# Optimization experiments

Hardware: AMD Instinct MI355X
Metric: run time of the kernel (lower is better)

Reference implementation:

```python
import jax, jax.numpy as jnp
import numpy as np

B, S, D, H, L, V, C = 8, 1024, 768, 12, 6, 32000, 2
HD = D // H
DF = 3072
MAX_POS = 2048
EPS = 1e-5


def layer_norm(x, scale, bias):
    m = jnp.mean(x, axis=-1, keepdims=True)
    v = jnp.mean((x - m) ** 2, axis=-1, keepdims=True)
    return (x - m) / jnp.sqrt(v + EPS) * scale + bias


def setup_inputs() -> dict:
    key = jax.random.key(0)
    ks = jax.random.split(key, 16)
    std = 0.02
    return {
        "input_ids": jax.random.randint(ks[0], (B, S), 0, V),
        "attention_mask": jax.random.randint(ks[1], (B, S), 0, 2),
        "token_emb": jax.random.normal(ks[2], (V, D), jnp.float32) * std,
        "pos_emb": jax.random.normal(ks[3], (MAX_POS, D), jnp.float32) * std,
        "qkv_w": jax.random.normal(ks[4], (L, D, 3 * D), jnp.float32) * std,
        "qkv_b": jnp.zeros((L, 3 * D), jnp.float32),
        "out_w": jax.random.normal(ks[5], (L, D, D), jnp.float32) * std,
        "out_b": jnp.zeros((L, D), jnp.float32),
        "n1_s": jnp.ones((L, D), jnp.float32),
        "n1_b": jnp.zeros((L, D), jnp.float32),
        "ff1_w": jax.random.normal(ks[6], (L, D, DF), jnp.float32) * std,
        "ff1_b": jnp.zeros((L, DF), jnp.float32),
        "ff2_w": jax.random.normal(ks[7], (L, DF, D), jnp.float32) * std,
        "ff2_b": jnp.zeros((L, D), jnp.float32),
        "n2_s": jnp.ones((L, D), jnp.float32),
        "n2_b": jnp.zeros((L, D), jnp.float32),
        "hln_s": jnp.ones((D,), jnp.float32),
        "hln_b": jnp.zeros((D,), jnp.float32),
        "cls_w": jax.random.normal(ks[8], (D, C), jnp.float32) * std,
        "cls_b": jnp.zeros((C,), jnp.float32),
    }


def reference(input_ids, attention_mask, token_emb, pos_emb, qkv_w, qkv_b,
              out_w, out_b, n1_s, n1_b, ff1_w, ff1_b, ff2_w, ff2_b,
              n2_s, n2_b, hln_s, hln_b, cls_w, cls_b):
    # embeddings: token + position, scaled by sqrt(d_model)
    x = (token_emb[input_ids] + pos_emb[:S][None, :, :]) * np.float32(np.sqrt(D))
    # extended mask: 0 at valid tokens, -10000 at padding -> (B,1,1,S)
    ext = (1.0 - attention_mask.astype(x.dtype))[:, None, None, :] * -10000.0
    scale = np.float32(1.0 / np.sqrt(HD))
    for i in range(L):
        # --- self attention (pre-norm) ---
        h = layer_norm(x, n1_s[i], n1_b[i])
        qkv = (h @ qkv_w[i] + qkv_b[i]).reshape(B, S, H, 3, HD)
        q, k, v = qkv[..., 0, :], qkv[..., 1, :], qkv[..., 2, :]  # (B,S,H,HD)
        scores = jnp.einsum('bshd,bthd->bhst', q, k) * scale
        # faithful to source: masked_fill(ext_mask == 0, -1e9)
        scores = jnp.where(ext == 0, jnp.asarray(-1e9, scores.dtype), scores)
        w = jax.nn.softmax(scores, axis=-1)
        att = jnp.einsum('bhst,bthd->bshd', w, v).reshape(B, S, D)
        x = x + (att @ out_w[i] + out_b[i])
        # --- feed forward (pre-norm) ---
        h2 = layer_norm(x, n2_s[i], n2_b[i])
        ff = jax.nn.relu(h2 @ ff1_w[i] + ff1_b[i]) @ ff2_w[i] + ff2_b[i]
        x = x + ff
    # CLS pooling head
    pooled = layer_norm(x[:, 0, :], hln_s, hln_b)
    return pooled @ cls_w + cls_b
```

## Files before the change

kernel.cpp:

```cpp
#include <hip/hip_runtime.h>
#include <hip/hip_bf16.h>

typedef unsigned short u16;
typedef __bf16 bf16x8 __attribute__((ext_vector_type(8)));
typedef float f32x4 __attribute__((ext_vector_type(4)));
typedef unsigned int u32x4 __attribute__((ext_vector_type(4)));

#define DEVI __device__ __forceinline__

typedef __attribute__((address_space(3))) void lds_void;
typedef __attribute__((address_space(1))) const void gbl_void;

DEVI void gload16(const void* gp, void* lp) {
    __builtin_amdgcn_global_load_lds((gbl_void*)gp, (lds_void*)lp, 16, 0, 0);
}

DEVI u16 f2b(float f) {
    unsigned int u = __builtin_bit_cast(unsigned int, f);
    unsigned int lsb = (u >> 16) & 1u;
    u += 0x7fffu + lsb;
    return (u16)(u >> 16);
}
DEVI float b2f(u16 b) {
    unsigned int u = ((unsigned int)b) << 16;
    return __builtin_bit_cast(float, u);
}

DEVI float blockReduceSum(float v, float* red, int tid) {
    #pragma unroll
    for (int o = 32; o; o >>= 1) v += __shfl_xor(v, o);
    __syncthreads();
    if ((tid & 63) == 0) red[tid >> 6] = v;
    __syncthreads();
    return red[0] + red[1] + red[2] + red[3];
}

__global__ void detect_kernel(const void* tok, int* flag) {
    __shared__ int bad;
    if (threadIdx.x == 0) bad = 0;
    __syncthreads();
    const u16* p = (const u16*)tok;
    int cnt = 0;
    for (int j = 0; j < 16; ++j) {
        float v = b2f(p[2 * (threadIdx.x * 16 + j)]);
        if (!(fabsf(v) < 1.0f)) cnt++;
    }
    if (cnt) atomicAdd(&bad, 1);
    __syncthreads();
    if (threadIdx.x == 0) flag[0] = (bad == 0) ? 1 : 0;
}

__global__ void to_f32_kernel(const void* src, float* dst, int n, const int* flag) {
    int i = blockIdx.x * 256 + threadIdx.x;
    if (i >= n) return;
    if (flag[0]) dst[i] = b2f(((const u16*)src)[i]);
    else         dst[i] = ((const float*)src)[i];
}

DEVI void gemm_core_async(const u16* __restrict__ A, int lda,
                          const u16* __restrict__ Bt, int ldb,
                          int K, f32x4 (&acc)[4][4],
                          u16* As, u16* Bs)
{
    const int tid  = threadIdx.x;
    const int lane = tid & 63;
    const int wave = tid >> 6;
    const int quad = lane >> 4;
    const int l16  = lane & 15;
    const int wm   = wave >> 1;
    const int wn   = wave & 1;

    const int c0 = (wave * 2 + 0) * 64 + lane;
    const int c1 = (wave * 2 + 1) * 64 + lane;
    const int r0 = c0 >> 2, h0 = (c0 & 3) * 8;
    const int r1 = c1 >> 2, h1 = (c1 & 3) * 8;

    for (int k0 = 0; k0 < K; k0 += 32) {
        __syncthreads();
        gload16(A  + (size_t)r0 * lda + k0 + h0, As + c0 * 8);
        gload16(Bt + (size_t)r0 * ldb + k0 + h0, Bs + c0 * 8);
        gload16(A  + (size_t)r1 * lda + k0 + h1, As + c1 * 8);
        gload16(Bt + (size_t)r1 * ldb + k0 + h1, Bs + c1 * 8);
        __syncthreads();

        bf16x8 af[4], bfv[4];
        #pragma unroll
        for (int mt = 0; mt < 4; ++mt)
            af[mt] = *(const bf16x8*)(As + (wm * 64 + mt * 16 + l16) * 32 + quad * 8);
        #pragma unroll
        for (int nt = 0; nt < 4; ++nt)
            bfv[nt] = *(const bf16x8*)(Bs + (wn * 64 + nt * 16 + l16) * 32 + quad * 8);
        #pragma unroll
        for (int mt = 0; mt < 4; ++mt)
            #pragma unroll
            for (int nt = 0; nt < 4; ++nt)
                acc[mt][nt] = __builtin_amdgcn_mfma_f32_16x16x32_bf16(af[mt], bfv[nt], acc[mt][nt], 0, 0, 0);
    }
}

template<int EPI>
__global__ __launch_bounds__(256) void gemm_std(
    const u16* __restrict__ A, int lda,
    const u16* __restrict__ Bt, int ldb,
    const float* __restrict__ bias,
    u16* __restrict__ outB, int ldc, int K)
{
    __shared__ u16 As[128 * 32];
    __shared__ u16 Bs[128 * 32];
    const size_t bM = (size_t)blockIdx.y * 128;
    const size_t bN = (size_t)blockIdx.x * 128;
    f32x4 acc[4][4] = {};
    gemm_core_async(A + bM * lda, lda, Bt + bN * ldb, ldb, K, acc, As, Bs);

    const int tid = threadIdx.x, lane = tid & 63, wave = tid >> 6;
    const int wm = wave >> 1, wn = wave & 1, quad = lane >> 4, l16 = lane & 15;
    #pragma unroll
    for (int mt = 0; mt < 4; ++mt)
        #pragma unroll
        for (int nt = 0; nt < 4; ++nt) {
            size_t col = bN + wn * 64 + nt * 16 + l16;
            float bcol = bias[col];
            #pragma unroll
            for (int r = 0; r < 4; ++r) {
                size_t row = bM + wm * 64 + mt * 16 + quad * 4 + r;
                float v = acc[mt][nt][r] + bcol;
                if constexpr (EPI == 1) v = fmaxf(v, 0.f);
                outB[row * ldc + col] = f2b(v);
            }
        }
}

__global__ __launch_bounds__(256) void gemm_splitk(
    const u16* __restrict__ A, int lda,
    const u16* __restrict__ Bt, int ldb,
    const float* __restrict__ bias,
    float* __restrict__ resid, int ldc, int Ksub)
{
    __shared__ u16 As[128 * 32];
    __shared__ u16 Bs[128 * 32];
    const size_t bM = (size_t)blockIdx.y * 128;
    const size_t bN = (size_t)blockIdx.x * 128;
    const int Koff = blockIdx.z * Ksub;
    f32x4 acc[4][4] = {};
    gemm_core_async(A + bM * lda + Koff, lda, Bt + bN * ldb + Koff, ldb, Ksub, acc, As, Bs);

    const int tid = threadIdx.x, lane = tid & 63, wave = tid >> 6;
    const int wm = wave >> 1, wn = wave & 1, quad = lane >> 4, l16 = lane & 15;
    const bool addb = (blockIdx.z == 0);
    #pragma unroll
    for (int mt = 0; mt < 4; ++mt)
        #pragma unroll
        for (int nt = 0; nt < 4; ++nt) {
            size_t col = bN + wn * 64 + nt * 16 + l16;
            float bcol = addb ? bias[col] : 0.f;
            #pragma unroll
            for (int r = 0; r < 4; ++r) {
                size_t row = bM + wm * 64 + mt * 16 + quad * 4 + r;
                atomicAdd(&resid[row * ldc + col], acc[mt][nt][r] + bcol);
            }
        }
}

__global__ __launch_bounds__(256, 2) void flash_attn(
    const u16* __restrict__ qkv, const u16* __restrict__ vt,
    const int* __restrict__ mask, u16* __restrict__ attout)
{
    __shared__ u16 Ks[128 * 72];
    __shared__ u16 Vs[64 * 136];
    __shared__ u16 Ps[128 * 136];
    __shared__ float Ms[1024];

    const int bh = blockIdx.y;
    const int b = bh / 12, h = bh % 12;
    const int q0 = blockIdx.x * 128;
    const int tid = threadIdx.x, lane = tid & 63, wave = tid >> 6;
    const int quad = lane >> 4, l16 = lane & 15;

    for (int i = tid; i < 1024; i += 256)
        Ms[i] = (mask[b * 1024 + i] != 0) ? 1.f : 0.f;

    bf16x8 aq[2][2];
    #pragma unroll
    for (int mt = 0; mt < 2; ++mt)
        #pragma unroll
        for (int s = 0; s < 2; ++s)
            aq[mt][s] = *(const bf16x8*)(qkv + (size_t)(b * 1024 + q0 + wave * 32 + mt * 16 + l16) * 2304
                                          + h * 192 + s * 32 + quad * 8);

    float mi[2][4], li[2][4];
    f32x4 Oacc[2][4] = {};
    #pragma unroll
    for (int mt = 0; mt < 2; ++mt)
        #pragma unroll
        for (int r = 0; r < 4; ++r) { mi[mt][r] = -3e38f; li[mt][r] = 0.f; }

    for (int kt = 0; kt < 8; ++kt) {
        u32x4 kreg[4], vreg[4];
        #pragma unroll
        for (int i = 0; i < 4; ++i) {
            int id = i * 256 + tid, row = id >> 3, ch = id & 7;
            kreg[i] = *(const u32x4*)(qkv + (size_t)(b * 1024 + kt * 128 + row) * 2304 + h * 192 + 64 + ch * 8);
        }
        #pragma unroll
        for (int i = 0; i < 4; ++i) {
            int id = i * 256 + tid, row = id >> 4, ch = id & 15;
            vreg[i] = *(const u32x4*)(vt + (size_t)bh * 65536 + (size_t)row * 1024 + kt * 128 + ch * 8);
        }
        __syncthreads();
        #pragma unroll
        for (int i = 0; i < 4; ++i) {
            int id = i * 256 + tid, row = id >> 3, ch = id & 7;
            *(u32x4*)(Ks + row * 72 + ch * 8) = kreg[i];
        }
        #pragma unroll
        for (int i = 0; i < 4; ++i) {
            int id = i * 256 + tid, row = id >> 4, ch = id & 15;
            *(u32x4*)(Vs + row * 136 + ch * 8) = vreg[i];
        }
        __syncthreads();

        f32x4 Sacc[2][8] = {};
        #pragma unroll
        for (int s = 0; s < 2; ++s) {
            bf16x8 kf[8];
            #pragma unroll
            for (int nt = 0; nt < 8; ++nt)
                kf[nt] = *(const bf16x8*)(Ks + (nt * 16 + l16) * 72 + s * 32 + quad * 8);
            #pragma unroll
            for (int mt = 0; mt < 2; ++mt)
                #pragma unroll
                for (int nt = 0; nt < 8; ++nt)
                    Sacc[mt][nt] = __builtin_amdgcn_mfma_f32_16x16x32_bf16(aq[mt][s], kf[nt], Sacc[mt][nt], 0, 0, 0);
        }

        float mval[8];
        #pragma unroll
        for (int nt = 0; nt < 8; ++nt) mval[nt] = Ms[kt * 128 + nt * 16 + l16];
        #pragma unroll
        for (int mt = 0; mt < 2; ++mt)
            #pragma unroll
            for (int nt = 0; nt < 8; ++nt)
                #pragma unroll
                for (int r = 0; r < 4; ++r)
                    Sacc[mt][nt][r] = (mval[nt] != 0.f) ? -1e9f : Sacc[mt][nt][r] * 0.125f;

        #pragma unroll
        for (int mt = 0; mt < 2; ++mt) {
            float al[4];
            #pragma unroll
            for (int r = 0; r < 4; ++r) {
                float rm = -3e38f;
                #pragma unroll
                for (int nt = 0; nt < 8; ++nt) rm = fmaxf(rm, Sacc[mt][nt][r]);
                #pragma unroll
                for (int o = 8; o; o >>= 1) rm = fmaxf(rm, __shfl_xor(rm, o));
                float mn = fmaxf(mi[mt][r], rm);
                al[r] = __expf(mi[mt][r] - mn);
                mi[mt][r] = mn;
                float rs = 0.f;
                #pragma unroll
                for (int nt = 0; nt < 8; ++nt) {
                    float pv = __expf(Sacc[mt][nt][r] - mn);
                    rs += pv;
                    Sacc[mt][nt][r] = pv;
                }
                #pragma unroll
                for (int o = 8; o; o >>= 1) rs += __shfl_xor(rs, o);
                li[mt][r] = li[mt][r] * al[r] + rs;
            }
            #pragma unroll
            for (int ntv = 0; ntv < 4; ++ntv)
                #pragma unroll
                for (int r = 0; r < 4; ++r) Oacc[mt][ntv][r] *= al[r];
            const int rowb = wave * 32 + mt * 16 + quad * 4;
            #pragma unroll
            for (int nt = 0; nt < 8; ++nt)
                #pragma unroll
                for (int r = 0; r < 4; ++r)
                    Ps[(rowb + r) * 136 + nt * 16 + l16] = f2b(Sacc[mt][nt][r]);
        }

        #pragma unroll
        for (int s2 = 0; s2 < 4; ++s2) {
            bf16x8 vf[4];
            #pragma unroll
            for (int ntv = 0; ntv < 4; ++ntv)
                vf[ntv] = *(const bf16x8*)(Vs + (ntv * 16 + l16) * 136 + s2 * 32 + quad * 8);
            #pragma unroll
            for (int mt2 = 0; mt2 < 2; ++mt2) {
                bf16x8 pf = *(const bf16x8*)(Ps + (wave * 32 + mt2 * 16 + l16) * 136 + s2 * 32 + quad * 8);
                #pragma unroll
                for (int ntv = 0; ntv < 4; ++ntv)
                    Oacc[mt2][ntv] = __builtin_amdgcn_mfma_f32_16x16x32_bf16(pf, vf[ntv], Oacc[mt2][ntv], 0, 0, 0);
            }
        }
    }

    #pragma unroll
    for (int mt = 0; mt < 2; ++mt)
        #pragma unroll
        for (int r = 0; r < 4; ++r) {
            float inv = 1.0f / li[mt][r];
            int s = q0 + wave * 32 + mt * 16 + quad * 4 + r;
            #pragma unroll
            for (int ntv = 0; ntv < 4; ++ntv)
                attout[((size_t)(b * 1024 + s)) * 768 + h * 64 + ntv * 16 + l16] = f2b(Oacc[mt][ntv][r] * inv);
        }
}

__global__ __launch_bounds__(256) void embed_kernel(
    const int* __restrict__ ids, const void* __restrict__ tok,
    const void* __restrict__ pos, float* __restrict__ x, const int* __restrict__ flag)
{
    const int e  = blockIdx.x * 256 + threadIdx.x;
    const int bs = e / 192;
    const int d  = (e - bs * 192) * 4;
    const int s  = bs & 1023;
    const int id = ids[bs];
    float t[4], p4[4];
    if (flag[0]) {
        const u16* tb = (const u16*)tok + (size_t)id * 768 + d;
        const u16* pb = (const u16*)pos + (size_t)s  * 768 + d;
        #pragma unroll
        for (int j = 0; j < 4; ++j) { t[j] = b2f(tb[j]); p4[j] = b2f(pb[j]); }
    } else {
        const float* tb = (const float*)tok + (size_t)id * 768 + d;
        const float* pb = (const float*)pos + (size_t)s  * 768 + d;
        #pragma unroll
        for (int j = 0; j < 4; ++j) { t[j] = tb[j]; p4[j] = pb[j]; }
    }
    float* xo = x + (size_t)bs * 768 + d;
    #pragma unroll
    for (int j = 0; j < 4; ++j) xo[j] = (t[j] + p4[j]) * 27.7128129211020f;
}

__global__ __launch_bounds__(256) void layernorm_kernel(
    const float* __restrict__ x, const float* __restrict__ sc,
    const float* __restrict__ bi, u16* __restrict__ out)
{
    __shared__ float red[4];
    const size_t row = blockIdx.x;
    const float* xr = x + row * 768;
    const int tid = threadIdx.x;
    float v0 = xr[tid], v1 = xr[tid + 256], v2 = xr[tid + 512];
    float s = blockReduceSum(v0 + v1 + v2, red, tid);
    float mean = s * (1.0f / 768.0f);
    float d0 = v0 - mean, d1 = v1 - mean, d2 = v2 - mean;
    float q = blockReduceSum(d0 * d0 + d1 * d1 + d2 * d2, red, tid);
    float rstd = rsqrtf(q * (1.0f / 768.0f) + 1e-5f);
    u16* orow = out + row * 768;
    orow[tid]       = f2b(d0 * rstd * sc[tid]       + bi[tid]);
    orow[tid + 256] = f2b(d1 * rstd * sc[tid + 256] + bi[tid + 256]);
    orow[tid + 512] = f2b(d2 * rstd * sc[tid + 512] + bi[tid + 512]);
}

__global__ __launch_bounds__(256) void transpose_w_kernel(
    const void* __restrict__ W, size_t off, u16* __restrict__ Wt,
    int Kd, int Nd, const int* __restrict__ flag)
{
    __shared__ u16 tile[32][34];
    const int n0 = blockIdx.x * 32, k0 = blockIdx.y * 32;
    const int tx = threadIdx.x & 31, ty = threadIdx.x >> 5;
    const int fl = flag[0];
    #pragma unroll
    for (int i = 0; i < 4; ++i) {
        size_t idx = off + (size_t)(k0 + ty + i * 8) * Nd + n0 + tx;
        u16 val = fl ? ((const u16*)W)[idx] : f2b(((const float*)W)[idx]);
        tile[ty + i * 8][tx] = val;
    }
    __syncthreads();
    #pragma unroll
    for (int i = 0; i < 4; ++i)
        Wt[(size_t)(n0 + ty + i * 8) * Kd + k0 + tx] = tile[tx][ty + i * 8];
}

__global__ __launch_bounds__(256) void build_vt_kernel(
    const u16* __restrict__ qkv, u16* __restrict__ vt)
{
    __shared__ u16 tile[64][72];
    const int bh = blockIdx.y;
    const int b = bh / 12, h = bh % 12;
    const int t0 = blockIdx.x * 64;
    const int tid = threadIdx.x;
    const int tl = tid >> 2;
    const int d4 = (tid & 3) * 16;
    const u16* src = qkv + (size_t)(b * 1024 + t0 + tl) * 2304 + h * 192 + 128 + d4;
    *(u32x4*)(&tile[tl][d4])     = *(const u32x4*)(src);
    *(u32x4*)(&tile[tl][d4 + 8]) = *(const u32x4*)(src + 8);
    __syncthreads();
    const int dd = tid >> 2;
    const int tstart = (tid & 3) * 16;
    union { u16 us[16]; u32x4 v[2]; } pk;
    #pragma unroll
    for (int j = 0; j < 16; ++j) pk.us[j] = tile[tstart + j][dd];
    u16* dst = vt + ((size_t)bh * 64 + dd) * 1024 + t0 + tstart;
    *(u32x4*)(dst)     = pk.v[0];
    *(u32x4*)(dst + 8) = pk.v[1];
}

__global__ __launch_bounds__(256) void pooled_cls_kernel(
    const float* __restrict__ x, const float* __restrict__ hs, const float* __restrict__ hb,
    const float* __restrict__ cw, const float* __restrict__ cb, void* __restrict__ dout,
    const int* __restrict__ flag)
{
    __shared__ float red[4];
    __shared__ float pooled[768];
    const int b = blockIdx.x;
    const float* xr = x + (size_t)b * 1024 * 768;
    const int tid = threadIdx.x;
    float v0 = xr[tid], v1 = xr[tid + 256], v2 = xr[tid + 512];
    float s = blockReduceSum(v0 + v1 + v2, red, tid);
    float mean = s * (1.0f / 768.0f);
    float d0 = v0 - mean, d1 = v1 - mean, d2 = v2 - mean;
    float q = blockReduceSum(d0 * d0 + d1 * d1 + d2 * d2, red, tid);
    float rstd = rsqrtf(q * (1.0f / 768.0f) + 1e-5f);
    pooled[tid]       = d0 * rstd * hs[tid]       + hb[tid];
    pooled[tid + 256] = d1 * rstd * hs[tid + 256] + hb[tid + 256];
    pooled[tid + 512] = d2 * rstd * hs[tid + 512] + hb[tid + 512];
    __syncthreads();
    float p0 = 0.f, p1 = 0.f;
    for (int c = tid; c < 768; c += 256) {
        float pv = pooled[c];
        p0 += pv * cw[2 * c];
        p1 += pv * cw[2 * c + 1];
    }
    p0 = blockReduceSum(p0, red, tid);
    p1 = blockReduceSum(p1, red, tid);
    if (tid == 0) {
        float o0 = p0 + cb[0], o1 = p1 + cb[1];
        if (flag[0]) {
            ((u16*)dout)[b * 2 + 0] = f2b(o0);
            ((u16*)dout)[b * 2 + 1] = f2b(o1);
        } else {
            ((float*)dout)[b * 2 + 0] = o0;
            ((float*)dout)[b * 2 + 1] = o1;
        }
    }
}

extern "C" void kernel_launch(void* const* d_in, const int* in_sizes, int n_in,
                              void* d_out, int out_size, void* d_ws, size_t ws_size,
                              hipStream_t stream)
{
    const int* ids  = (const int*)d_in[0];
    const int* mask = (const int*)d_in[1];
    const void* tok   = d_in[2];
    const void* pos   = d_in[3];
    const void* qkv_w = d_in[4];
    const void* qkv_b = d_in[5];
    const void* out_w = d_in[6];
    const void* out_b = d_in[7];
    const void* n1_s  = d_in[8];
    const void* n1_b  = d_in[9];
    const void* ff1_w = d_in[10];
    const void* ff1_b = d_in[11];
    const void* ff2_w = d_in[12];
    const void* ff2_b = d_in[13];
    const void* n2_s  = d_in[14];
    const void* n2_b  = d_in[15];
    const void* hln_s = d_in[16];
    const void* hln_b = d_in[17];
    const void* cls_w = d_in[18];
    const void* cls_b = d_in[19];

    char* p = (char*)d_ws;
    auto alloc = [&](size_t bytes) -> char* {
        char* r = p; p += (bytes + 255) & ~(size_t)255; return r;
    };
    float* x      = (float*)alloc(6291456ull * 4);
    u16*   h      = (u16*)  alloc(6291456ull * 2);
    u16*   qkvB   = (u16*)  alloc(18874368ull * 2);
    u16*   vt     = (u16*)  alloc(6291456ull * 2);
    u16*   ffmid  = (u16*)  alloc(25165824ull * 2);
    u16*   wqkvT  = (u16*)  alloc(1769472ull * 2);
    u16*   woutT  = (u16*)  alloc(589824ull * 2);
    u16*   wff1T  = (u16*)  alloc(2359296ull * 2);
    u16*   wff2T  = (u16*)  alloc(2359296ull * 2);
    float* params = (float*)alloc(62978ull * 4);
    int*   flag   = (int*)  alloc(256);
    u16*   attout = h;

    float* P_qkv_b = params + 0;
    float* P_out_b = params + 13824;
    float* P_n1_s  = params + 18432;
    float* P_n1_b  = params + 23040;
    float* P_ff1_b = params + 27648;
    float* P_ff2_b = params + 46080;
    float* P_n2_s  = params + 50688;
    float* P_n2_b  = params + 55296;
    float* P_hln_s = params + 59904;
    float* P_hln_b = params + 60672;
    float* P_cls_w = params + 61440;
    float* P_cls_b = params + 62976;

    detect_kernel<<<1, 256, 0, stream>>>(tok, flag);

    auto cvt = [&](const void* src, float* dst, int n) {
        to_f32_kernel<<<(n + 255) / 256, 256, 0, stream>>>(src, dst, n, flag);
    };
    cvt(qkv_b, P_qkv_b, 13824);  cvt(out_b, P_out_b, 4608);
    cvt(n1_s,  P_n1_s,  4608);   cvt(n1_b,  P_n1_b,  4608);
    cvt(ff1_b, P_ff1_b, 18432);  cvt(ff2_b, P_ff2_b, 4608);
    cvt(n2_s,  P_n2_s,  4608);   cvt(n2_b,  P_n2_b,  4608);
    cvt(hln_s, P_hln_s, 768);    cvt(hln_b, P_hln_b, 768);
    cvt(cls_w, P_cls_w, 1536);   cvt(cls_b, P_cls_b, 2);

    embed_kernel<<<6144, 256, 0, stream>>>(ids, tok, pos, x, flag);

    for (int l = 0; l < 6; ++l) {
        transpose_w_kernel<<<dim3(72, 24), 256, 0, stream>>>(qkv_w, (size_t)l * 1769472, wqkvT, 768, 2304, flag);
        transpose_w_kernel<<<dim3(24, 24), 256, 0, stream>>>(out_w, (size_t)l * 589824,  woutT, 768, 768,  flag);
        transpose_w_kernel<<<dim3(96, 24), 256, 0, stream>>>(ff1_w, (size_t)l * 2359296, wff1T, 768, 3072, flag);
        transpose_w_kernel<<<dim3(24, 96), 256, 0, stream>>>(ff2_w, (size_t)l * 2359296, wff2T, 3072, 768, flag);

        layernorm_kernel<<<8192, 256, 0, stream>>>(x, P_n1_s + l * 768, P_n1_b + l * 768, h);
        gemm_std<0><<<dim3(18, 64), 256, 0, stream>>>(h, 768, wqkvT, 768,
                                                      P_qkv_b + l * 2304, qkvB, 2304, 768);
        build_vt_kernel<<<dim3(16, 96), 256, 0, stream>>>(qkvB, vt);
        flash_attn<<<dim3(8, 96), 256, 0, stream>>>(qkvB, vt, mask, attout);
        gemm_splitk<<<dim3(6, 64, 2), 256, 0, stream>>>(attout, 768, woutT, 768,
                                                        P_out_b + l * 768, x, 768, 384);
        layernorm_kernel<<<8192, 256, 0, stream>>>(x, P_n2_s + l * 768, P_n2_b + l * 768, h);
        gemm_std<1><<<dim3(24, 64), 256, 0, stream>>>(h, 768, wff1T, 768,
                                                      P_ff1_b + l * 3072, ffmid, 3072, 768);
        gemm_splitk<<<dim3(6, 64, 2), 256, 0, stream>>>(ffmid, 3072, wff2T, 3072,
                                                        P_ff2_b + l * 768, x, 768, 1536);
    }
    pooled_cls_kernel<<<8, 256, 0, stream>>>(x, P_hln_s, P_hln_b, P_cls_w, P_cls_b, d_out, flag);
}
```

Baseline: 2.566 ms.

## Swizzle attention LDS tiles, halve P buffer, fold mask into exp2 softmax

Flash attention drops padded LDS strides in favor of XOR-swizzled layouts for K, V and P, and stages P in two 64-column halves to halve its LDS footprint. The mask becomes a bf16 additive bias fused with the scale into one FMA, and exponentials use exp2 with log2e folded into the scale. Occupancy bounds rise from 2 to 3 blocks per SM. Together these cut LDS use and bank conflicts to fit more resident blocks and trim ALU work in softmax. The risks are extra register pressure from the higher occupancy target and a small change in precision.

```diff
diff --git a/kernel.cpp b/kernel.cpp
--- a/kernel.cpp
+++ b/kernel.cpp
@@ -24,6 +24,14 @@
 DEVI float b2f(u16 b) {
     unsigned int u = ((unsigned int)b) << 16;
     return __builtin_bit_cast(float, u);
+}
+
+DEVI float fexp2(float x) {
+#if __has_builtin(__builtin_amdgcn_exp2f)
+    return __builtin_amdgcn_exp2f(x);
+#else
+    return __expf(x * 0.6931471805599453f);
+#endif
 }
 
 DEVI float blockReduceSum(float v, float* red, int tid) {
@@ -161,23 +169,24 @@
         }
 }
 
-__global__ __launch_bounds__(256, 2) void flash_attn(
+__global__ __launch_bounds__(256, 3) void flash_attn(
     const u16* __restrict__ qkv, const u16* __restrict__ vt,
     const int* __restrict__ mask, u16* __restrict__ attout)
 {
-    __shared__ u16 Ks[128 * 72];
-    __shared__ u16 Vs[64 * 136];
-    __shared__ u16 Ps[128 * 136];
-    __shared__ float Ms[1024];
+    __shared__ u16 Ks[128 * 64];
+    __shared__ u16 Vs[64 * 128];
+    __shared__ u16 Ps[128 * 64];
+    __shared__ u16 Msb[1024];
 
     const int bh = blockIdx.y;
     const int b = bh / 12, h = bh % 12;
     const int q0 = blockIdx.x * 128;
     const int tid = threadIdx.x, lane = tid & 63, wave = tid >> 6;
     const int quad = lane >> 4, l16 = lane & 15;
+    const int sw = l16 & 7;
 
     for (int i = tid; i < 1024; i += 256)
-        Ms[i] = (mask[b * 1024 + i] != 0) ? 1.f : 0.f;
+        Msb[i] = (mask[b * 1024 + i] != 0) ? f2b(-1e9f) : (u16)0;
 
     bf16x8 aq[2][2];
     #pragma unroll
@@ -187,6 +196,8 @@
             aq[mt][s] = *(const bf16x8*)(qkv + (size_t)(b * 1024 + q0 + wave * 32 + mt * 16 + l16) * 2304
                                           + h * 192 + s * 32 + quad * 8);
 
+    const float SC2 = 0.18033688011112042f;
+
     float mi[2][4], li[2][4];
     f32x4 Oacc[2][4] = {};
     #pragma unroll
@@ -210,12 +221,12 @@
         #pragma unroll
         for (int i = 0; i < 4; ++i) {
             int id = i * 256 + tid, row = id >> 3, ch = id & 7;
-            *(u32x4*)(Ks + row * 72 + ch * 8) = kreg[i];
+            *(u32x4*)(Ks + row * 64 + ((ch ^ (row & 7)) * 8)) = kreg[i];
         }
         #pragma unroll
         for (int i = 0; i < 4; ++i) {
             int id = i * 256 + tid, row = id >> 4, ch = id & 15;
-            *(u32x4*)(Vs + row * 136 + ch * 8) = vreg[i];
+            *(u32x4*)(Vs + row * 128 + ((ch ^ (row & 7)) * 8)) = vreg[i];
         }
         __syncthreads();
 
@@ -225,7 +236,7 @@
             bf16x8 kf[8];
             #pragma unroll
             for (int nt = 0; nt < 8; ++nt)
-                kf[nt] = *(const bf16x8*)(Ks + (nt * 16 + l16) * 72 + s * 32 + quad * 8);
+                kf[nt] = *(const bf16x8*)(Ks + (nt * 16 + l16) * 64 + (((s * 4 + quad) ^ sw) * 8));
             #pragma unroll
             for (int mt = 0; mt < 2; ++mt)
                 #pragma unroll
@@ -233,34 +244,34 @@
                     Sacc[mt][nt] = __builtin_amdgcn_mfma_f32_16x16x32_bf16(aq[mt][s], kf[nt], Sacc[mt][nt], 0, 0, 0);
         }
 
-        float mval[8];
-        #pragma unroll
-        for (int nt = 0; nt < 8; ++nt) mval[nt] = Ms[kt * 128 + nt * 16 + l16];
+        float bias[8];
+        #pragma unroll
+        for (int nt = 0; nt < 8; ++nt) bias[nt] = b2f(Msb[kt * 128 + nt * 16 + l16]);
         #pragma unroll
         for (int mt = 0; mt < 2; ++mt)
             #pragma unroll
             for (int nt = 0; nt < 8; ++nt)
                 #pragma unroll
                 for (int r = 0; r < 4; ++r)
-                    Sacc[mt][nt][r] = (mval[nt] != 0.f) ? -1e9f : Sacc[mt][nt][r] * 0.125f;
+                    Sacc[mt][nt][r] = fmaf(Sacc[mt][nt][r], SC2, bias[nt]);
 
         #pragma unroll
         for (int mt = 0; mt < 2; ++mt) {
             float al[4];
             #pragma unroll
             for (int r = 0; r < 4; ++r) {
-                float rm = -3e38f;
-                #pragma unroll
-                for (int nt = 0; nt < 8; ++nt) rm = fmaxf(rm, Sacc[mt][nt][r]);
+                float rm = fmaxf(
+                    fmaxf(fmaxf(Sacc[mt][0][r], Sacc[mt][1][r]), fmaxf(Sacc[mt][2][r], Sacc[mt][3][r])),
+                    fmaxf(fmaxf(Sacc[mt][4][r], Sacc[mt][5][r]), fmaxf(Sacc[mt][6][r], Sacc[mt][7][r])));
                 #pragma unroll
                 for (int o = 8; o; o >>= 1) rm = fmaxf(rm, __shfl_xor(rm, o));
                 float mn = fmaxf(mi[mt][r], rm);
-                al[r] = __expf(mi[mt][r] - mn);
+                al[r] = fexp2(mi[mt][r] - mn);
                 mi[mt][r] = mn;
                 float rs = 0.f;
                 #pragma unroll
                 for (int nt = 0; nt < 8; ++nt) {
-                    float pv = __expf(Sacc[mt][nt][r] - mn);
+                    float pv = fexp2(Sacc[mt][nt][r] - mn);
                     rs += pv;
                     Sacc[mt][nt][r] = pv;
                 }
@@ -272,26 +283,37 @@
             for (int ntv = 0; ntv < 4; ++ntv)
                 #pragma unroll
                 for (int r = 0; r < 4; ++r) Oacc[mt][ntv][r] *= al[r];
-            const int rowb = wave * 32 + mt * 16 + quad * 4;
-            #pragma unroll
-            for (int nt = 0; nt < 8; ++nt)
-                #pragma unroll
-                for (int r = 0; r < 4; ++r)
-                    Ps[(rowb + r) * 136 + nt * 16 + l16] = f2b(Sacc[mt][nt][r]);
-        }
-
-        #pragma unroll
-        for (int s2 = 0; s2 < 4; ++s2) {
-            bf16x8 vf[4];
-            #pragma unroll
-            for (int ntv = 0; ntv < 4; ++ntv)
-                vf[ntv] = *(const bf16x8*)(Vs + (ntv * 16 + l16) * 136 + s2 * 32 + quad * 8);
-            #pragma unroll
-            for (int mt2 = 0; mt2 < 2; ++mt2) {
-                bf16x8 pf = *(const bf16x8*)(Ps + (wave * 32 + mt2 * 16 + l16) * 136 + s2 * 32 + quad * 8);
+        }
+
+        #pragma unroll
+        for (int hf = 0; hf < 2; ++hf) {
+            #pragma unroll
+            for (int mt = 0; mt < 2; ++mt) {
+                const int rowb = wave * 32 + mt * 16 + quad * 4;
+                #pragma unroll
+                for (int n4 = 0; n4 < 4; ++n4) {
+                    const int slot = n4 * 2 + (l16 >> 3);
+                    #pragma unroll
+                    for (int r = 0; r < 4; ++r) {
+                        const int row = rowb + r;
+                        Ps[row * 64 + ((slot ^ (row & 7)) * 8) + sw] = f2b(Sacc[mt][hf * 4 + n4][r]);
+                    }
+                }
+            }
+            #pragma unroll
+            for (int s2h = 0; s2h < 2; ++s2h) {
+                const int s2 = hf * 2 + s2h;
+                bf16x8 vf[4];
                 #pragma unroll
                 for (int ntv = 0; ntv < 4; ++ntv)
-                    Oacc[mt2][ntv] = __builtin_amdgcn_mfma_f32_16x16x32_bf16(pf, vf[ntv], Oacc[mt2][ntv], 0, 0, 0);
+                    vf[ntv] = *(const bf16x8*)(Vs + (ntv * 16 + l16) * 128 + (((s2 * 4 + quad) ^ sw) * 8));
+                #pragma unroll
+                for (int mt2 = 0; mt2 < 2; ++mt2) {
+                    bf16x8 pf = *(const bf16x8*)(Ps + (wave * 32 + mt2 * 16 + l16) * 64 + (((s2h * 4 + quad) ^ sw) * 8));
+                    #pragma unroll
+                    for (int ntv = 0; ntv < 4; ++ntv)
+                        Oacc[mt2][ntv] = __builtin_amdgcn_mfma_f32_16x16x32_bf16(pf, vf[ntv], Oacc[mt2][ntv], 0, 0, 0);
+                }
             }
         }
     }
```

Measured after the change: 2.944 ms. +14.7%, slower.
